# Kernel optimization log

Hardware: AMD Instinct MI355X
Metric: run time of the kernel (lower is better)

The kernel has to match this reference:

```python
import jax, jax.numpy as jnp
import numpy as np

B, S, E, H = 4, 2048, 1280, 5


def setup_inputs() -> dict:
    key = jax.random.key(0)
    ks = jax.random.split(key, 5)
    scale = 1.0 / np.sqrt(E)
    return {
        "x": jax.random.normal(ks[0], (B, S, E), dtype=jnp.float32),
        "Wq": jax.random.normal(ks[1], (E, E), dtype=jnp.float32) * scale,
        "Wk": jax.random.normal(ks[2], (E, E), dtype=jnp.float32) * scale,
        "Wv": jax.random.normal(ks[3], (E, E), dtype=jnp.float32) * scale,
        "Wu": jax.random.normal(ks[4], (E, E), dtype=jnp.float32) * scale,
        "bu": jnp.zeros((E,), dtype=jnp.float32),
    }


def reference(x, Wq, Wk, Wv, Wu, bu):
    b, s_len, e = x.shape
    h = H
    d = e // h
    # torch nn.Linear: y = x @ W.T
    q = (x @ Wq.T).reshape(b, s_len, h, d).transpose(0, 2, 1, 3)  # b h s d
    k = (x @ Wk.T).reshape(b, s_len, h, d).transpose(0, 2, 1, 3)
    v = (x @ Wv.T).reshape(b, s_len, h, d).transpose(0, 2, 1, 3)
    # NOTE: original scales by sqrt(emb_dim), not sqrt(head_dim)
    scores = jnp.einsum("bhqd,bhkd->bhqk", q, k) / (e ** 0.5)
    # 'upper diag matrix' mask: strictly-upper-triangular positions -> -inf (causal)
    causal = jnp.triu(jnp.ones((s_len, s_len), dtype=bool), k=1)
    scores = jnp.where(causal[None, None], jnp.float32(-jnp.inf), scores)
    att = jax.nn.softmax(scores, axis=-1)
    out = jnp.einsum("bhqk,bhkd->bhqd", att, v)
    out = out.transpose(0, 2, 1, 3).reshape(b, s_len, e)
    return out @ Wu.T + bu
```

## Files before the change

kernel.cpp:

```cpp
#include <hip/hip_runtime.h>
#include <hip/hip_bf16.h>
#include <stdint.h>

#define B_  4
#define S_  2048
#define E_  1280
#define H_  5
#define D_  256
#define BH_ 20
#define M_  8192
#define K_  1280

#define SCALE_ 0.027950849718747372f

typedef __attribute__((ext_vector_type(8))) __bf16 bf16x8;
typedef __attribute__((ext_vector_type(4))) float  f32x4;

__device__ __forceinline__ ushort f2bf(float f) {
  union { float f; uint32_t u; } v; v.f = f;
  return (ushort)((v.u + 0x7FFFu + ((v.u >> 16) & 1u)) >> 16);
}

typedef const __attribute__((address_space(1))) void* gas_cvp;
typedef __attribute__((address_space(3))) void*       las_vp;

__device__ __forceinline__ void glds16(const void* g, void* l) {
  __builtin_amdgcn_global_load_lds((gas_cvp)g, (las_vp)l, 16, 0, 0);
}

__global__ void cvt5_kernel(const float4* __restrict__ s0, const float4* __restrict__ s1,
                            const float4* __restrict__ s2, const float4* __restrict__ s3,
                            const float4* __restrict__ s4,
                            ushort4* __restrict__ d0, ushort4* __restrict__ d1,
                            ushort4* __restrict__ d2, ushort4* __restrict__ d3,
                            ushort4* __restrict__ d4, int nx, int nw) {
  int seg = blockIdx.y;
  const float4* s = (seg == 0) ? s0 : (seg == 1) ? s1 : (seg == 2) ? s2 : (seg == 3) ? s3 : s4;
  ushort4*       d = (seg == 0) ? d0 : (seg == 1) ? d1 : (seg == 2) ? d2 : (seg == 3) ? d3 : d4;
  int n4 = (seg == 0) ? nx : nw;
  int i = blockIdx.x * blockDim.x + threadIdx.x;
  int stride = gridDim.x * blockDim.x;
  for (; i < n4; i += stride) {
    float4 v = s[i];
    ushort4 u;
    u.x = f2bf(v.x); u.y = f2bf(v.y); u.z = f2bf(v.z); u.w = f2bf(v.w);
    d[i] = u;
  }
}

__global__ __launch_bounds__(256, 2)
void gemm_qkv(const ushort* __restrict__ A,
              const ushort* __restrict__ Wq, const ushort* __restrict__ Wk,
              const ushort* __restrict__ Wv,
              ushort* __restrict__ Qo, ushort* __restrict__ Ko, ushort* __restrict__ Vo)
{
  __shared__ __align__(16) ushort Abuf[128 * 64];
  __shared__ __align__(16) ushort Bbuf[128 * 64];
  const int tid  = threadIdx.x;
  const int lane = tid & 63;
  const int wid  = tid >> 6;
  const int m0 = blockIdx.x * 128;
  const int which = blockIdx.y / 10;
  const int n0 = (blockIdx.y % 10) * 128;
  const ushort* W = (which == 0) ? Wq : (which == 1) ? Wk : Wv;
  const int wr = (wid >> 1) * 64;
  const int wc = (wid & 1) * 64;

  f32x4 acc[4][4] = {};
  const int soff = wid * 4096 + lane * 16;

  for (int kk = 0; kk < K_; kk += 64) {
    __syncthreads();
#pragma unroll
    for (int i = 0; i < 4; ++i) {
      int off = soff + i * 1024;
      int row = off >> 7;
      int c8  = (off >> 4) & 7;
      int s8  = c8 ^ (row & 7);
      glds16(A + (size_t)(m0 + row) * K_ + kk + s8 * 8,
             (char*)Abuf + wid * 4096 + i * 1024);
      glds16(W + (size_t)(n0 + row) * K_ + kk + s8 * 8,
             (char*)Bbuf + wid * 4096 + i * 1024);
    }
    __syncthreads();
#pragma unroll
    for (int kt = 0; kt < 2; ++kt) {
      bf16x8 af[4], bfr[4];
#pragma unroll
      for (int mf = 0; mf < 4; ++mf) {
        int row  = wr + mf * 16 + (lane & 15);
        int byte = (row << 7) + kt * 64 + ((lane >> 4) << 4);
        af[mf] = *(const bf16x8*)((const char*)Abuf + (byte ^ ((row & 7) << 4)));
      }
#pragma unroll
      for (int nf = 0; nf < 4; ++nf) {
        int row  = wc + nf * 16 + (lane & 15);
        int byte = (row << 7) + kt * 64 + ((lane >> 4) << 4);
        bfr[nf] = *(const bf16x8*)((const char*)Bbuf + (byte ^ ((row & 7) << 4)));
      }
#pragma unroll
      for (int mf = 0; mf < 4; ++mf)
#pragma unroll
        for (int nf = 0; nf < 4; ++nf)
          acc[mf][nf] = __builtin_amdgcn_mfma_f32_16x16x32_bf16(
              af[mf], bfr[nf], acc[mf][nf], 0, 0, 0);
    }
  }

#pragma unroll
  for (int mf = 0; mf < 4; ++mf) {
#pragma unroll
    for (int nf = 0; nf < 4; ++nf) {
      int mbase = m0 + wr + mf * 16 + ((lane >> 4) << 2);
      int n     = n0 + wc + nf * 16 + (lane & 15);
      int h = n >> 8, dd = n & 255;
      if (which == 0) {
#pragma unroll
        for (int r = 0; r < 4; ++r) {
          int m = mbase + r;
          Qo[((size_t)(((m >> 11) * H_ + h) * S_ + (m & 2047))) * D_ + dd] =
              f2bf(acc[mf][nf][r] * SCALE_);
        }
      } else if (which == 1) {
#pragma unroll
        for (int r = 0; r < 4; ++r) {
          int m = mbase + r;
          Ko[((size_t)(((m >> 11) * H_ + h) * S_ + (m & 2047))) * D_ + dd] =
              f2bf(acc[mf][nf][r]);
        }
      } else {
        size_t idx = ((size_t)((mbase >> 11) * H_ + h) * D_ + dd) * S_ + (mbase & 2047);
        ushort4 pk;
        pk.x = f2bf(acc[mf][nf][0]);
        pk.y = f2bf(acc[mf][nf][1]);
        pk.z = f2bf(acc[mf][nf][2]);
        pk.w = f2bf(acc[mf][nf][3]);
        *(ushort4*)(Vo + idx) = pk;
      }
    }
  }
}

__global__ __launch_bounds__(256, 2)
void gemm_out(const ushort* __restrict__ A, const ushort* __restrict__ W,
              float* __restrict__ OF, const float* __restrict__ bias)
{
  __shared__ __align__(16) ushort Abuf[128 * 64];
  __shared__ __align__(16) ushort Bbuf[128 * 64];
  const int tid  = threadIdx.x;
  const int lane = tid & 63;
  const int wid  = tid >> 6;
  const int m0 = blockIdx.x * 128;
  const int n0 = blockIdx.y * 128;
  const int wr = (wid >> 1) * 64;
  const int wc = (wid & 1) * 64;

  f32x4 acc[4][4] = {};
  const int soff = wid * 4096 + lane * 16;

  for (int kk = 0; kk < K_; kk += 64) {
    __syncthreads();
#pragma unroll
    for (int i = 0; i < 4; ++i) {
      int off = soff + i * 1024;
      int row = off >> 7;
      int c8  = (off >> 4) & 7;
      int s8  = c8 ^ (row & 7);
      glds16(A + (size_t)(m0 + row) * K_ + kk + s8 * 8,
             (char*)Abuf + wid * 4096 + i * 1024);
      glds16(W + (size_t)(n0 + row) * K_ + kk + s8 * 8,
             (char*)Bbuf + wid * 4096 + i * 1024);
    }
    __syncthreads();
#pragma unroll
    for (int kt = 0; kt < 2; ++kt) {
      bf16x8 af[4], bfr[4];
#pragma unroll
      for (int mf = 0; mf < 4; ++mf) {
        int row  = wr + mf * 16 + (lane & 15);
        int byte = (row << 7) + kt * 64 + ((lane >> 4) << 4);
        af[mf] = *(const bf16x8*)((const char*)Abuf + (byte ^ ((row & 7) << 4)));
      }
#pragma unroll
      for (int nf = 0; nf < 4; ++nf) {
        int row  = wc + nf * 16 + (lane & 15);
        int byte = (row << 7) + kt * 64 + ((lane >> 4) << 4);
        bfr[nf] = *(const bf16x8*)((const char*)Bbuf + (byte ^ ((row & 7) << 4)));
      }
#pragma unroll
      for (int mf = 0; mf < 4; ++mf)
#pragma unroll
        for (int nf = 0; nf < 4; ++nf)
          acc[mf][nf] = __builtin_amdgcn_mfma_f32_16x16x32_bf16(
              af[mf], bfr[nf], acc[mf][nf], 0, 0, 0);
    }
  }

#pragma unroll
  for (int mf = 0; mf < 4; ++mf) {
#pragma unroll
    for (int nf = 0; nf < 4; ++nf) {
      int mbase = m0 + wr + mf * 16 + ((lane >> 4) << 2);
      int n     = n0 + wc + nf * 16 + (lane & 15);
      float bv = bias[n];
#pragma unroll
      for (int r = 0; r < 4; ++r)
        OF[(size_t)(mbase + r) * E_ + n] = acc[mf][nf][r] + bv;
    }
  }
}

__global__ __launch_bounds__(256, 2)
void flash_attn_kernel(const ushort* __restrict__ Q, const ushort* __restrict__ Kg,
                       const ushort* __restrict__ Vt, ushort* __restrict__ AO)
{
  __shared__ __align__(16) ushort Kbuf[2][32 * 256];
  __shared__ __align__(16) ushort Vbuf[2][256 * 32];
  __shared__ __align__(16) char   Pbuf[4 * 16 * 80];

  const int lane = threadIdx.x & 63;
  const int wid  = threadIdx.x >> 6;
  const int l15  = lane & 15;
  const int l4   = lane >> 4;

  const int id  = blockIdx.x;
  const int idp = (id & 7) * 80 + (id >> 3);
  const int bh  = idp >> 5;
  const int tq  = 31 - (idp & 31);
  const int q0w = tq * 64 + wid * 16;

  const ushort* Qb = Q  + (size_t)bh * S_ * D_;
  const ushort* Kb = Kg + (size_t)bh * S_ * D_;
  const ushort* Vb = Vt + (size_t)bh * D_ * S_;

  bf16x8 bq[8];
  {
    const ushort* qrow = Qb + (size_t)(q0w + l15) * D_ + l4 * 8;
#pragma unroll
    for (int kt = 0; kt < 8; ++kt) bq[kt] = *(const bf16x8*)(qrow + kt * 32);
  }

  f32x4 o[16] = {};
  float m_s = -1e30f, l_s = 0.f;

  char* Pw = Pbuf + wid * 1280;
  const int nt = 2 * tq + 2;

#define STAGE_KV(bufi, kvbase)                                                \
  do {                                                                        \
    _Pragma("unroll")                                                         \
    for (int i_ = 0; i_ < 4; ++i_) {                                          \
      int off_ = wid * 4096 + i_ * 1024 + lane * 16;                          \
      int rK_  = off_ >> 9;                                                   \
      int s8_  = ((off_ >> 4) & 31) ^ (rK_ & 7);                              \
      glds16(Kb + (size_t)((kvbase) + rK_) * D_ + s8_ * 8,                    \
             (char*)Kbuf[bufi] + wid * 4096 + i_ * 1024);                     \
      int rV_  = off_ >> 6;                                                   \
      int qv_  = ((off_ >> 4) & 3) ^ ((rV_ >> 1) & 3);                        \
      glds16(Vb + (size_t)rV_ * S_ + (kvbase) + (qv_ << 3),                   \
             (char*)Vbuf[bufi] + wid * 4096 + i_ * 1024);                     \
    }                                                                         \
  } while (0)

  STAGE_KV(0, 0);
  __syncthreads();

  const int vsw = (l4 ^ ((l15 >> 1) & 3)) << 4;

  int cur = 0;
  for (int t = 0; t < nt; ++t) {
    const int kv0 = t * 32;
    if (t + 1 < nt) STAGE_KV(cur ^ 1, kv0 + 32);

    if (kv0 <= q0w + 15) {
      f32x4 sacc[2] = {};
      const char* kb = (const char*)Kbuf[cur];
      __builtin_amdgcn_s_setprio(1);
#pragma unroll
      for (int kt = 0; kt < 8; ++kt) {
#pragma unroll
        for (int h2 = 0; h2 < 2; ++h2) {
          int row  = h2 * 16 + l15;
          int byte = (row << 9) + kt * 64 + (l4 << 4);
          bf16x8 kf = *(const bf16x8*)(kb + (byte ^ ((row & 7) << 4)));
          sacc[h2] = __builtin_amdgcn_mfma_f32_16x16x32_bf16(kf, bq[kt], sacc[h2], 0, 0, 0);
        }
      }
      __builtin_amdgcn_s_setprio(0);

      const bool msk = (kv0 + 31 > q0w);
      float sv[2][4];
#pragma unroll
      for (int h2 = 0; h2 < 2; ++h2)
#pragma unroll
        for (int r = 0; r < 4; ++r) {
          float s = sacc[h2][r];
          if (msk && (kv0 + h2 * 16 + l4 * 4 + r > q0w + l15)) s = -1e30f;
          sv[h2][r] = s;
        }
      float pm = sv[0][0];
#pragma unroll
      for (int h2 = 0; h2 < 2; ++h2)
#pragma unroll
        for (int r = 0; r < 4; ++r) pm = fmaxf(pm, sv[h2][r]);
      pm = fmaxf(pm, __shfl_xor(pm, 16, 64));
      pm = fmaxf(pm, __shfl_xor(pm, 32, 64));

      if (__any(pm > m_s + 8.f)) {
        float mn = fmaxf(m_s, pm);
        float alpha = __expf(m_s - mn);
        m_s = mn;
#pragma unroll
        for (int h2 = 0; h2 < 2; ++h2)
#pragma unroll
          for (int r = 0; r < 4; ++r) sv[h2][r] = __expf(sv[h2][r] - m_s);
        float rs = 0.f;
#pragma unroll
        for (int h2 = 0; h2 < 2; ++h2)
#pragma unroll
          for (int r = 0; r < 4; ++r) rs += sv[h2][r];
        rs += __shfl_xor(rs, 16, 64);
        rs += __shfl_xor(rs, 32, 64);
        l_s = l_s * alpha + rs;
        float al[4];
#pragma unroll
        for (int r = 0; r < 4; ++r)
          al[r] = __shfl(alpha, (lane & 48) + ((lane & 48) >> 2) + r, 64);
#pragma unroll
        for (int nf = 0; nf < 16; ++nf)
#pragma unroll
          for (int r = 0; r < 4; ++r) o[nf][r] *= al[r];
      } else {
#pragma unroll
        for (int h2 = 0; h2 < 2; ++h2)
#pragma unroll
          for (int r = 0; r < 4; ++r) sv[h2][r] = __expf(sv[h2][r] - m_s);
        float rs = 0.f;
#pragma unroll
        for (int h2 = 0; h2 < 2; ++h2)
#pragma unroll
          for (int r = 0; r < 4; ++r) rs += sv[h2][r];
        rs += __shfl_xor(rs, 16, 64);
        rs += __shfl_xor(rs, 32, 64);
        l_s += rs;
      }

      ushort4 w0, w1;
      w0.x = f2bf(sv[0][0]); w0.y = f2bf(sv[0][1]); w0.z = f2bf(sv[0][2]); w0.w = f2bf(sv[0][3]);
      w1.x = f2bf(sv[1][0]); w1.y = f2bf(sv[1][1]); w1.z = f2bf(sv[1][2]); w1.w = f2bf(sv[1][3]);
      *(ushort4*)(Pw + l15 * 80 + l4 * 8)      = w0;
      *(ushort4*)(Pw + l15 * 80 + 32 + l4 * 8) = w1;
      bf16x8 pa = *(const bf16x8*)(Pw + l15 * 80 + l4 * 16);

      const char* vb = (const char*)Vbuf[cur];
      __builtin_amdgcn_s_setprio(1);
#pragma unroll
      for (int nf = 0; nf < 16; ++nf) {
        bf16x8 bv = *(const bf16x8*)(vb + ((nf * 16 + l15) << 6) + vsw);
        o[nf] = __builtin_amdgcn_mfma_f32_16x16x32_bf16(pa, bv, o[nf], 0, 0, 0);
      }
      __builtin_amdgcn_s_setprio(0);
    }

    __syncthreads();
    cur ^= 1;
  }
#undef STAGE_KV

  float linv = 1.0f / l_s;
  float inv[4];
#pragma unroll
  for (int r = 0; r < 4; ++r)
    inv[r] = __shfl(linv, (lane & 48) + ((lane & 48) >> 2) + r, 64);
  int b = bh / H_, h = bh % H_;
  const int dd0 = h * D_;
#pragma unroll
  for (int nf = 0; nf < 16; ++nf) {
    int dd = dd0 + nf * 16 + l15;
#pragma unroll
    for (int r = 0; r < 4; ++r) {
      int s = q0w + l4 * 4 + r;
      AO[(size_t)(b * S_ + s) * E_ + dd] = f2bf(o[nf][r] * inv[r]);
    }
  }
}

extern "C" void kernel_launch(void* const* d_in, const int* in_sizes, int n_in,
                              void* d_out, int out_size, void* d_ws, size_t ws_size,
                              hipStream_t stream) {
  const float* x  = (const float*)d_in[0];
  const float* Wq = (const float*)d_in[1];
  const float* Wk = (const float*)d_in[2];
  const float* Wv = (const float*)d_in[3];
  const float* Wu = (const float*)d_in[4];
  const float* bu = (const float*)d_in[5];

  char* ws = (char*)d_ws;
  ushort* xbf = (ushort*)(ws + 0);
  ushort* Wqb = (ushort*)(ws + 20971520);
  ushort* Wkb = (ushort*)(ws + 24248320);
  ushort* Wvb = (ushort*)(ws + 27525120);
  ushort* Wub = (ushort*)(ws + 30801920);
  ushort* Qw  = (ushort*)(ws + 34078720);
  ushort* Kw  = (ushort*)(ws + 55050240);
  ushort* Vtw = (ushort*)(ws + 76021760);
  ushort* AOw = (ushort*)(ws + 96993280);

  cvt5_kernel<<<dim3(1024, 5), 256, 0, stream>>>(
      (const float4*)x, (const float4*)Wq, (const float4*)Wk,
      (const float4*)Wv, (const float4*)Wu,
      (ushort4*)xbf, (ushort4*)Wqb, (ushort4*)Wkb, (ushort4*)Wvb, (ushort4*)Wub,
      M_ * K_ / 4, E_ * E_ / 4);

  gemm_qkv<<<dim3(M_ / 128, 30), 256, 0, stream>>>(xbf, Wqb, Wkb, Wvb, Qw, Kw, Vtw);

  flash_attn_kernel<<<640, 256, 0, stream>>>(Qw, Kw, Vtw, AOw);

  gemm_out<<<dim3(M_ / 128, E_ / 128), 256, 0, stream>>>(AOw, Wub, (float*)d_out, bu);
}
```

Baseline: 356.9 us.

## Double-buffer LDS tiles in QKV and output projection GEMMs

Both projection GEMMs now keep two shared-memory buffers for the A and W tiles. Each iteration issues the global-to-LDS copies for the next K slice before running the MFMA work on the current slice, with one barrier per iteration instead of two. The aim is to hide global load latency behind matrix math. In exchange, shared-memory use per block doubles to 64 KB, which could limit occupancy, and the barrier at the end of each iteration still waits for the prefetch to land.

```diff
diff --git a/kernel.cpp b/kernel.cpp
--- a/kernel.cpp
+++ b/kernel.cpp
@@ -54,8 +54,8 @@
               const ushort* __restrict__ Wv,
               ushort* __restrict__ Qo, ushort* __restrict__ Ko, ushort* __restrict__ Vo)
 {
-  __shared__ __align__(16) ushort Abuf[128 * 64];
-  __shared__ __align__(16) ushort Bbuf[128 * 64];
+  __shared__ __align__(16) ushort Abuf[2][128 * 64];
+  __shared__ __align__(16) ushort Bbuf[2][128 * 64];
   const int tid  = threadIdx.x;
   const int lane = tid & 63;
   const int wid  = tid >> 6;
@@ -69,20 +69,26 @@
   f32x4 acc[4][4] = {};
   const int soff = wid * 4096 + lane * 16;
 
+#define STAGE_AB(bufi, kk)                                                    \
+  do {                                                                        \
+    _Pragma("unroll")                                                         \
+    for (int i_ = 0; i_ < 4; ++i_) {                                          \
+      int off_ = soff + i_ * 1024;                                            \
+      int row_ = off_ >> 7;                                                   \
+      int s8_  = ((off_ >> 4) & 7) ^ (row_ & 7);                              \
+      glds16(A + (size_t)(m0 + row_) * K_ + (kk) + s8_ * 8,                   \
+             (char*)Abuf[bufi] + wid * 4096 + i_ * 1024);                     \
+      glds16(W + (size_t)(n0 + row_) * K_ + (kk) + s8_ * 8,                   \
+             (char*)Bbuf[bufi] + wid * 4096 + i_ * 1024);                     \
+    }                                                                         \
+  } while (0)
+
+  STAGE_AB(0, 0);
+  __syncthreads();
+
+  int cur = 0;
   for (int kk = 0; kk < K_; kk += 64) {
-    __syncthreads();
-#pragma unroll
-    for (int i = 0; i < 4; ++i) {
-      int off = soff + i * 1024;
-      int row = off >> 7;
-      int c8  = (off >> 4) & 7;
-      int s8  = c8 ^ (row & 7);
-      glds16(A + (size_t)(m0 + row) * K_ + kk + s8 * 8,
-             (char*)Abuf + wid * 4096 + i * 1024);
-      glds16(W + (size_t)(n0 + row) * K_ + kk + s8 * 8,
-             (char*)Bbuf + wid * 4096 + i * 1024);
-    }
-    __syncthreads();
+    if (kk + 64 < K_) STAGE_AB(cur ^ 1, kk + 64);
 #pragma unroll
     for (int kt = 0; kt < 2; ++kt) {
       bf16x8 af[4], bfr[4];
@@ -90,13 +96,13 @@
       for (int mf = 0; mf < 4; ++mf) {
         int row  = wr + mf * 16 + (lane & 15);
         int byte = (row << 7) + kt * 64 + ((lane >> 4) << 4);
-        af[mf] = *(const bf16x8*)((const char*)Abuf + (byte ^ ((row & 7) << 4)));
+        af[mf] = *(const bf16x8*)((const char*)Abuf[cur] + (byte ^ ((row & 7) << 4)));
       }
 #pragma unroll
       for (int nf = 0; nf < 4; ++nf) {
         int row  = wc + nf * 16 + (lane & 15);
         int byte = (row << 7) + kt * 64 + ((lane >> 4) << 4);
-        bfr[nf] = *(const bf16x8*)((const char*)Bbuf + (byte ^ ((row & 7) << 4)));
+        bfr[nf] = *(const bf16x8*)((const char*)Bbuf[cur] + (byte ^ ((row & 7) << 4)));
       }
 #pragma unroll
       for (int mf = 0; mf < 4; ++mf)
@@ -105,7 +111,10 @@
           acc[mf][nf] = __builtin_amdgcn_mfma_f32_16x16x32_bf16(
               af[mf], bfr[nf], acc[mf][nf], 0, 0, 0);
     }
-  }
+    __syncthreads();
+    cur ^= 1;
+  }
+#undef STAGE_AB
 
 #pragma unroll
   for (int mf = 0; mf < 4; ++mf) {
@@ -145,8 +154,8 @@
 void gemm_out(const ushort* __restrict__ A, const ushort* __restrict__ W,
               float* __restrict__ OF, const float* __restrict__ bias)
 {
-  __shared__ __align__(16) ushort Abuf[128 * 64];
-  __shared__ __align__(16) ushort Bbuf[128 * 64];
+  __shared__ __align__(16) ushort Abuf[2][128 * 64];
+  __shared__ __align__(16) ushort Bbuf[2][128 * 64];
   const int tid  = threadIdx.x;
   const int lane = tid & 63;
   const int wid  = tid >> 6;
@@ -158,20 +167,26 @@
   f32x4 acc[4][4] = {};
   const int soff = wid * 4096 + lane * 16;
 
+#define STAGE_AB(bufi, kk)                                                    \
+  do {                                                                        \
+    _Pragma("unroll")                                                         \
+    for (int i_ = 0; i_ < 4; ++i_) {                                          \
+      int off_ = soff + i_ * 1024;                                            \
+      int row_ = off_ >> 7;                                                   \
+      int s8_  = ((off_ >> 4) & 7) ^ (row_ & 7);                              \
+      glds16(A + (size_t)(m0 + row_) * K_ + (kk) + s8_ * 8,                   \
+             (char*)Abuf[bufi] + wid * 4096 + i_ * 1024);                     \
+      glds16(W + (size_t)(n0 + row_) * K_ + (kk) + s8_ * 8,                   \
+             (char*)Bbuf[bufi] + wid * 4096 + i_ * 1024);                     \
+    }                                                                         \
+  } while (0)
+
+  STAGE_AB(0, 0);
+  __syncthreads();
+
+  int cur = 0;
   for (int kk = 0; kk < K_; kk += 64) {
-    __syncthreads();
-#pragma unroll
-    for (int i = 0; i < 4; ++i) {
-      int off = soff + i * 1024;
-      int row = off >> 7;
-      int c8  = (off >> 4) & 7;
-      int s8  = c8 ^ (row & 7);
-      glds16(A + (size_t)(m0 + row) * K_ + kk + s8 * 8,
-             (char*)Abuf + wid * 4096 + i * 1024);
-      glds16(W + (size_t)(n0 + row) * K_ + kk + s8 * 8,
-             (char*)Bbuf + wid * 4096 + i * 1024);
-    }
-    __syncthreads();
+    if (kk + 64 < K_) STAGE_AB(cur ^ 1, kk + 64);
 #pragma unroll
     for (int kt = 0; kt < 2; ++kt) {
       bf16x8 af[4], bfr[4];
@@ -179,13 +194,13 @@
       for (int mf = 0; mf < 4; ++mf) {
         int row  = wr + mf * 16 + (lane & 15);
         int byte = (row << 7) + kt * 64 + ((lane >> 4) << 4);
-        af[mf] = *(const bf16x8*)((const char*)Abuf + (byte ^ ((row & 7) << 4)));
+        af[mf] = *(const bf16x8*)((const char*)Abuf[cur] + (byte ^ ((row & 7) << 4)));
       }
 #pragma unroll
       for (int nf = 0; nf < 4; ++nf) {
         int row  = wc + nf * 16 + (lane & 15);
         int byte = (row << 7) + kt * 64 + ((lane >> 4) << 4);
-        bfr[nf] = *(const bf16x8*)((const char*)Bbuf + (byte ^ ((row & 7) << 4)));
+        bfr[nf] = *(const bf16x8*)((const char*)Bbuf[cur] + (byte ^ ((row & 7) << 4)));
       }
 #pragma unroll
       for (int mf = 0; mf < 4; ++mf)
@@ -194,7 +209,10 @@
           acc[mf][nf] = __builtin_amdgcn_mfma_f32_16x16x32_bf16(
               af[mf], bfr[nf], acc[mf][nf], 0, 0, 0);
     }
-  }
+    __syncthreads();
+    cur ^= 1;
+  }
+#undef STAGE_AB
 
 #pragma unroll
   for (int mf = 0; mf < 4; ++mf) {
```

After: 393.2 us. +10.2%, slower.
